# Performance work log

Hardware: AMD Instinct MI355X
Metric: run time of the kernel (lower is better)

Reference implementation:

```python
import jax, jax.numpy as jnp
import numpy as np

N = 4096   # atoms
B = 64     # structures in batch
K = 128    # k-vectors per structure
E = 256    # emb_size_atom
D = 8      # downprojection_size
NUM_HIDDEN = 3


def _silu(x):
    return x * jax.nn.sigmoid(x)


def _residual(x, W):
    # ResidualLayer: two bias-free Dense(E,E) with SiLU, plus skip
    y = _silu(x @ W[0].T)
    y = _silu(y @ W[1].T)
    return x + y


def setup_inputs() -> dict:
    key = jax.random.key(0)
    ks = jax.random.split(key, 10)
    h = jax.random.normal(ks[0], (N, E), jnp.float32)
    x = jax.random.uniform(ks[1], (N, 3), jnp.float32) * 10.0  # Angstrom-scale positions
    k = jax.random.normal(ks[2], (B, K, 3), jnp.float32)
    batch_seg = jnp.sort(jax.random.randint(ks[3], (N,), 0, B))
    sc = 1.0 / np.sqrt(E)
    W_pre = jax.random.normal(ks[4], (2, E, E), jnp.float32) * sc        # pre_residual
    W_down = jax.random.normal(ks[5], (D, K), jnp.float32) / np.sqrt(K)  # shared downprojection (D,K)
    W_up = jax.random.normal(ks[6], (E, D), jnp.float32) / np.sqrt(D)    # up (E,D)
    W0 = jax.random.normal(ks[7], (E, E), jnp.float32) * sc              # first dense of ewald_layers
    W_res = jax.random.normal(ks[8], (NUM_HIDDEN, 2, E, E), jnp.float32) * sc
    return {"h": h, "x": x, "k": k, "batch_seg": batch_seg, "num_batch": B,
            "W_pre": W_pre, "W_down": W_down, "W_up": W_up, "W0": W0, "W_res": W_res}


def reference(h, x, k, batch_seg, num_batch, W_pre, W_down, W_up, W0, W_res):
    hres = _residual(h, W_pre)                       # (N,E)
    # dot products of atom positions with their structure's k-vectors
    dot = jnp.einsum('nkd,nd->nk', k[batch_seg], x)  # (N,K); sinc_damping == 1 (use_pbc)
    c, s = jnp.cos(dot), jnp.sin(dot)
    # structure factors: scatter-sum over atoms within each structure
    sf_real = jax.ops.segment_sum(hres[:, None, :] * c[:, :, None], batch_seg,
                                  num_segments=num_batch)  # (B,K,E)
    sf_imag = jax.ops.segment_sum(hres[:, None, :] * s[:, :, None], batch_seg,
                                  num_segments=num_batch)  # (B,K,E)
    # low-rank learned Fourier-space filter (use_pbc branch)
    kfilter = (W_up @ W_down).T                      # (K,E)
    # re-project filtered structure factors back to atoms
    h_update = 0.01 * jnp.sum(
        (sf_real * kfilter)[batch_seg] * c[:, :, None]
        + (sf_imag * kfilter)[batch_seg] * s[:, :, None], axis=1)  # (N,E)
    # ewald_layers update MLP: Dense + num_hidden residual blocks
    hu = _silu(h_update @ W0.T)
    for i in range(NUM_HIDDEN):
        hu = _residual(hu, W_res[i])
    return hu, dot
```

## Files before the change

### kernel.cpp

```cpp
#include <hip/hip_runtime.h>

#define NN 4096
#define BB 64
#define KK 128
#define EE 256
#define HTS 4352
#define CSR 4224
#define PCAP 160
#define YTS 264
#define ZTS 20

typedef unsigned short u16;
typedef __bf16 bhalf;
typedef bhalf bhalf8 __attribute__((ext_vector_type(8)));
typedef float floatx4 __attribute__((ext_vector_type(4)));

__device__ __forceinline__ float b2f(u16 u) {
  union { unsigned int i; float f; } v; v.i = ((unsigned int)u) << 16; return v.f;
}
__device__ __forceinline__ u16 f2b(float f) {
  union { float f; unsigned int i; } v; v.f = f;
  unsigned int r = (v.i + 0x7FFFu + ((v.i >> 16) & 1u)) >> 16;
  return (u16)r;
}
__device__ __forceinline__ float silu_f(float v) {
  return v / (1.f + __expf(-v));
}


__global__ __launch_bounds__(256) void p1_k(
    const float* __restrict__ h, const float* __restrict__ Wpre,
    const float* __restrict__ W0, const float* __restrict__ Wres,
    const float* __restrict__ Wup, const float* __restrict__ Wdn,
    const int* __restrict__ bs, const float* __restrict__ x,
    const float* __restrict__ kvec,
    u16* __restrict__ hb, u16* __restrict__ wpre, u16* __restrict__ w0b,
    u16* __restrict__ wrb, float* __restrict__ kft, u16* __restrict__ csb,
    int* __restrict__ seg, float* __restrict__ dout)
{
  int bid = blockIdx.x, tid = threadIdx.x;
  if (bid < 4096)      { int i = bid * 256 + tid;          hb[i]   = f2b(h[i]); }
  else if (bid < 6400) {
    int wb = bid - 4096;
    int mat = wb >> 8;
    int o = (wb & 255) * 256 + tid;
    int i = o & 7, lane = (o >> 3) & 63, k = (o >> 9) & 7, nt = o >> 12;
    int r = lane & 15, q = lane >> 4;
    int src = (nt * 16 + r) * 256 + q * 8 + k * 32 + i;
    const float* S; u16* D;
    if (mat < 2)      { S = Wpre + mat * 65536;       D = wpre + mat * 65536; }
    else if (mat == 2){ S = W0;                       D = w0b; }
    else              { S = Wres + (mat - 3) * 65536; D = wrb + (mat - 3) * 65536; }
    D[o] = f2b(S[src]);
  }
  else if (bid < 6528) {
    int i = (bid - 6400) * 256 + tid;
    int e = i >> 7, kk = i & 127;
    float a = 0.f;
#pragma unroll
    for (int d = 0; d < 8; ++d) a += Wup[e * 8 + d] * Wdn[d * KK + kk];
    kft[i] = a;
  } else if (bid < 6656) {
    int i = (bid - 6528) * 256 + tid;
    csb[4096 * 256 + i] = 0;
  } else if (bid == 6656) {
    int b = tid;
    if (b <= BB) {
      int lo = 0, hi = NN;
      while (lo < hi) { int mid = (lo + hi) >> 1; if (bs[mid] < b) lo = mid + 1; else hi = mid; }
      seg[b] = lo;
    }
  } else {
    int i = (bid - 6657) * 256 + tid;
    int n = i >> 7, kk = i & 127;
    int b = bs[n];
    const float* kp = kvec + (b * KK + kk) * 3;
    const float* xp = x + n * 3;
    float d = kp[0] * xp[0] + kp[1] * xp[1] + kp[2] * xp[2];
    float sv, cv;
    sincosf(d, &sv, &cv);
    dout[i] = d;
    csb[(n << 8) + kk] = f2b(cv);
    csb[(n << 8) + 128 + kk] = f2b(sv);
  }
}

__global__ __launch_bounds__(256) void p2_k(
    const u16* __restrict__ X, const u16* __restrict__ Wa, const u16* __restrict__ Wb,
    const float* __restrict__ hskip, u16* __restrict__ ht,
    const u16* __restrict__ csb, const int* __restrict__ seg, u16* __restrict__ ctb)
{
  __shared__ u16 sh[8256];
  if (blockIdx.x < 256) {
    const int lane = threadIdx.x & 63, wv = threadIdx.x >> 6;
    const int m0 = blockIdx.x * 16;
    const int n0 = wv * 64;
    const int r = lane & 15, q = lane >> 4;
    const int lane8 = lane * 8;
    const u16* Ap = X + (m0 + r) * EE + q * 8;
    floatx4 acc[4];
#pragma unroll
    for (int t = 0; t < 4; ++t) acc[t] = (floatx4){0.f, 0.f, 0.f, 0.f};
#pragma unroll
    for (int k = 0; k < 8; ++k) {
      bhalf8 av = *(const bhalf8*)(Ap + k * 32);
#pragma unroll
      for (int t = 0; t < 4; ++t) {
        bhalf8 bv = *(const bhalf8*)(Wa + ((wv * 4 + t) * 8 + k) * 512 + lane8);
        acc[t] = __builtin_amdgcn_mfma_f32_16x16x32_bf16(av, bv, acc[t], 0, 0, 0);
      }
    }
#pragma unroll
    for (int t = 0; t < 4; ++t) {
      int col = n0 + t * 16 + r;
#pragma unroll
      for (int i = 0; i < 4; ++i)
        sh[(q * 4 + i) * YTS + col] = f2b(silu_f(acc[t][i]));
    }
    __syncthreads();
#pragma unroll
    for (int t = 0; t < 4; ++t) acc[t] = (floatx4){0.f, 0.f, 0.f, 0.f};
#pragma unroll
    for (int k = 0; k < 8; ++k) {
      bhalf8 av = *(const bhalf8*)(&sh[r * YTS + q * 8 + k * 32]);
#pragma unroll
      for (int t = 0; t < 4; ++t) {
        bhalf8 bv = *(const bhalf8*)(Wb + ((wv * 4 + t) * 8 + k) * 512 + lane8);
        acc[t] = __builtin_amdgcn_mfma_f32_16x16x32_bf16(av, bv, acc[t], 0, 0, 0);
      }
    }
    __syncthreads();
#pragma unroll
    for (int t = 0; t < 4; ++t) {
      int col = n0 + t * 16 + r;
#pragma unroll
      for (int i = 0; i < 4; ++i) {
        int g = m0 + q * 4 + i;
        float v = silu_f(acc[t][i]) + hskip[g * EE + col];
        sh[col * ZTS + q * 4 + i] = f2b(v);
      }
    }
    __syncthreads();
    int e = threadIdx.x;
    const uint2* src = (const uint2*)&sh[e * ZTS];
    uint2* dst = (uint2*)(ht + e * HTS + m0);
#pragma unroll
    for (int i = 0; i < 4; ++i) dst[i] = src[i];
  } else {
    int bid2 = blockIdx.x - 256;
    int b = bid2 / 5, p0 = (bid2 % 5) * 32, t = threadIdx.x;
    int s0 = seg[b], s1 = seg[b + 1];
    int abase = s0 & ~7;
#pragma unroll
    for (int it = 0; it < 32; ++it) {
      int idx = it * 256 + t;
      int pl = idx >> 8, j = idx & 255;
      int n = abase + p0 + pl;
      u16 v = 0;
      if (n >= s0 && n < s1) v = csb[(n << 8) | j];
      sh[pl * 258 + j] = v;
    }
    __syncthreads();
    unsigned w[16];
#pragma unroll
    for (int i = 0; i < 16; ++i) {
      unsigned lo = sh[(2 * i) * 258 + t];
      unsigned hi = sh[(2 * i + 1) * 258 + t];
      w[i] = lo | (hi << 16);
    }
    uint4* dst = (uint4*)(ctb + ((b << 8) + t) * PCAP + p0);
#pragma unroll
    for (int i = 0; i < 4; ++i) {
      uint4 u; u.x = w[4*i]; u.y = w[4*i+1]; u.z = w[4*i+2]; u.w = w[4*i+3];
      dst[i] = u;
    }
  }
}

__global__ __launch_bounds__(256) void sf_k(
    const u16* __restrict__ ht, const u16* __restrict__ ctb,
    const float* __restrict__ kft, const int* __restrict__ seg, u16* __restrict__ F)
{
  const int lane = threadIdx.x & 63;
  const int wv = threadIdx.x >> 6;
  const int b = blockIdx.x;
  const int e0 = blockIdx.y * 128 + wv * 32;
  const int j0 = blockIdx.z * 64;
  const int r = lane & 15, q = lane >> 4;
  const int abase = seg[b] & ~7;
  const int phi = seg[b + 1] - abase;
  const u16* Ap = ht + (e0 + r) * HTS + abase + q * 8;
  const u16* Bp = ctb + ((b << 8) + j0 + r) * PCAP + q * 8;
  floatx4 acc[2][4];
#pragma unroll
  for (int m = 0; m < 2; ++m)
#pragma unroll
    for (int t = 0; t < 4; ++t) acc[m][t] = (floatx4){0.f, 0.f, 0.f, 0.f};
  for (int p0 = 0; p0 < phi; p0 += 32) {
    bhalf8 a0 = *(const bhalf8*)(Ap + p0);
    bhalf8 a1 = *(const bhalf8*)(Ap + 16 * HTS + p0);
#pragma unroll
    for (int t = 0; t < 4; ++t) {
      bhalf8 bv = *(const bhalf8*)(Bp + t * 16 * PCAP + p0);
      acc[0][t] = __builtin_amdgcn_mfma_f32_16x16x32_bf16(a0, bv, acc[0][t], 0, 0, 0);
      acc[1][t] = __builtin_amdgcn_mfma_f32_16x16x32_bf16(a1, bv, acc[1][t], 0, 0, 0);
    }
  }
#pragma unroll
  for (int m = 0; m < 2; ++m)
#pragma unroll
    for (int t = 0; t < 4; ++t) {
      int col = j0 + t * 16 + r;
      int kk = col & 127;
#pragma unroll
      for (int i = 0; i < 4; ++i) {
        int row = e0 + m * 16 + q * 4 + i;
        F[((b << 8) + row) * 256 + col] = f2b(acc[m][t][i] * kft[row * KK + kk]);
      }
    }
}

__device__ __forceinline__ void stage2(
    const u16* __restrict__ As, const u16* __restrict__ W,
    u16* __restrict__ Ad, const u16* __restrict__ Ask,
    float* __restrict__ outg, int R0, int c0, int r, int q, int wv, int lane8)
{
  bhalf8 a[8];
#pragma unroll
  for (int k = 0; k < 8; ++k)
    a[k] = *(const bhalf8*)(As + r * YTS + q * 8 + k * 32);
  bhalf8 bf[8][2];
#pragma unroll
  for (int k = 0; k < 8; ++k) {
#pragma unroll
    for (int t = 0; t < 2; ++t)
      bf[k][t] = *(const bhalf8*)(W + ((wv * 2 + t) * 8 + k) * 512 + lane8);
  }
  floatx4 acc[2];
  acc[0] = (floatx4){0.f, 0.f, 0.f, 0.f};
  acc[1] = (floatx4){0.f, 0.f, 0.f, 0.f};
#pragma unroll
  for (int k = 0; k < 8; ++k) {
    acc[0] = __builtin_amdgcn_mfma_f32_16x16x32_bf16(a[k], bf[k][0], acc[0], 0, 0, 0);
    acc[1] = __builtin_amdgcn_mfma_f32_16x16x32_bf16(a[k], bf[k][1], acc[1], 0, 0, 0);
  }
#pragma unroll
  for (int t = 0; t < 2; ++t) {
    int col = c0 + t * 16 + r;
#pragma unroll
    for (int i = 0; i < 4; ++i) {
      int row = q * 4 + i;
      float v = silu_f(acc[t][i]);
      if (Ask) v += b2f(Ask[row * YTS + col]);
      if (outg) outg[(R0 + row) * EE + col] = v;
      else      Ad[row * YTS + col] = f2b(v);
    }
  }
}

__global__ __launch_bounds__(512) void tail_k(
    const u16* __restrict__ csb, const u16* __restrict__ F,
    const int* __restrict__ bs, const int* __restrict__ seg,
    const u16* __restrict__ w0b, const u16* __restrict__ wrb,
    float* __restrict__ out)
{
  __shared__ u16 A0[16 * YTS], A1[16 * YTS];
  const int R0 = blockIdx.x * 16;
  const int lane = threadIdx.x & 63, wv = threadIdx.x >> 6;
  const int r = lane & 15, q = lane >> 4;
  const int c0 = wv * 32;
  const int lane8 = lane * 8;
  {
    const u16* Ap = csb + (R0 + r) * 256 + q * 8;
    bhalf8 a[8];
#pragma unroll
    for (int k = 0; k < 8; ++k) a[k] = *(const bhalf8*)(Ap + k * 32);
    int s = bs[R0];
    while (true) {
      const u16* Bp = F + ((s << 8) + c0 + r) * 256 + q * 8;
      bhalf8 bf[8][2];
#pragma unroll
      for (int k = 0; k < 8; ++k) {
        bf[k][0] = *(const bhalf8*)(Bp + k * 32);
        bf[k][1] = *(const bhalf8*)(Bp + 16 * 256 + k * 32);
      }
      floatx4 acc[2];
      acc[0] = (floatx4){0.f, 0.f, 0.f, 0.f};
      acc[1] = (floatx4){0.f, 0.f, 0.f, 0.f};
#pragma unroll
      for (int k = 0; k < 8; ++k) {
        acc[0] = __builtin_amdgcn_mfma_f32_16x16x32_bf16(a[k], bf[k][0], acc[0], 0, 0, 0);
        acc[1] = __builtin_amdgcn_mfma_f32_16x16x32_bf16(a[k], bf[k][1], acc[1], 0, 0, 0);
      }
      int lo = seg[s] - R0;     if (lo < 0)  lo = 0;
      int hi = seg[s + 1] - R0; if (hi > 16) hi = 16;
#pragma unroll
      for (int t = 0; t < 2; ++t) {
        int col = c0 + t * 16 + r;
#pragma unroll
        for (int i = 0; i < 4; ++i) {
          int row = q * 4 + i;
          if (row >= lo && row < hi)
            A0[row * YTS + col] = f2b(0.01f * acc[t][i]);
        }
      }
      if (seg[s + 1] >= R0 + 16) break;
      ++s;
    }
  }
  __syncthreads();
  stage2(A0, w0b,               A1, nullptr, nullptr, R0, c0, r, q, wv, lane8);
  __syncthreads();
  stage2(A1, wrb + 0 * EE * EE, A0, nullptr, nullptr, R0, c0, r, q, wv, lane8);
  __syncthreads();
  stage2(A0, wrb + 1 * EE * EE, A1, A1,      nullptr, R0, c0, r, q, wv, lane8);
  __syncthreads();
  stage2(A1, wrb + 2 * EE * EE, A0, nullptr, nullptr, R0, c0, r, q, wv, lane8);
  __syncthreads();
  stage2(A0, wrb + 3 * EE * EE, A1, A1,      nullptr, R0, c0, r, q, wv, lane8);
  __syncthreads();
  stage2(A1, wrb + 4 * EE * EE, A0, nullptr, nullptr, R0, c0, r, q, wv, lane8);
  __syncthreads();
  stage2(A0, wrb + 5 * EE * EE, nullptr, A1, out,     R0, c0, r, q, wv, lane8);
}

extern "C" void kernel_launch(void* const* d_in, const int* in_sizes, int n_in,
                              void* d_out, int out_size, void* d_ws, size_t ws_size,
                              hipStream_t stream) {
  const float* h    = (const float*)d_in[0];
  const float* x    = (const float*)d_in[1];
  const float* kv   = (const float*)d_in[2];
  const int*   bs   = (const int*)d_in[3];
  const float* Wpre = (const float*)d_in[5];
  const float* Wdn  = (const float*)d_in[6];
  const float* Wup  = (const float*)d_in[7];
  const float* W0   = (const float*)d_in[8];
  const float* Wres = (const float*)d_in[9];
  float* out = (float*)d_out;

  float* kft = (float*)d_ws;
  int*   seg = (int*)(kft + EE * KK);
  u16* hb   = (u16*)(seg + 128);
  u16* wpre = hb + NN * EE;
  u16* w0b  = wpre + 2 * EE * EE;
  u16* wrb  = w0b + EE * EE;
  u16* csb  = wrb + 6 * EE * EE;
  u16* ctb  = csb + CSR * 256;
  u16* ht   = ctb + BB * 256 * PCAP;
  u16* F    = ht + 256 * HTS;

  p1_k<<<8705, 256, 0, stream>>>(h, Wpre, W0, Wres, Wup, Wdn, bs, x, kv,
                                 hb, wpre, w0b, wrb, kft, csb, seg,
                                 out + NN * EE);
  p2_k<<<576, 256, 0, stream>>>(hb, wpre, wpre + EE * EE, h, ht, csb, seg, ctb);
  sf_k<<<dim3(BB, 2, 4), 256, 0, stream>>>(ht, ctb, kft, seg, F);
  tail_k<<<256, 512, 0, stream>>>(csb, F, bs, seg, w0b, wrb, out);
}
```

Before: 125.1 us.

## Fuse h bf16 conversion into GEMM load; double tail row tile and prefetch weights

The separate pass that converts h to bf16 is removed, and p2_k now reads fp32 h and converts it in registers while loading the GEMM operand. The tail kernel processes 32 rows per block instead of 16, so each weight fragment is reused across two M-tiles. The next layer's weights are also prefetched into registers while the current layer's MFMAs run. The trade-offs are higher register pressure, half as many tail blocks (128) for the GPU's CUs, and an extra fp32 read of h in p2.

Measured after the change: 129.3 us. +3.3%, slower.

```diff
diff --git a/kernel.cpp b/kernel.cpp
--- a/kernel.cpp
+++ b/kernel.cpp
@@ -26,24 +26,29 @@
 __device__ __forceinline__ float silu_f(float v) {
   return v / (1.f + __expf(-v));
 }
+__device__ __forceinline__ bhalf8 ld8f(const float* __restrict__ p) {
+  float4 f0 = *(const float4*)p;
+  float4 f1 = *(const float4*)(p + 4);
+  union { bhalf8 v; u16 s[8]; } u;
+  u.s[0] = f2b(f0.x); u.s[1] = f2b(f0.y); u.s[2] = f2b(f0.z); u.s[3] = f2b(f0.w);
+  u.s[4] = f2b(f1.x); u.s[5] = f2b(f1.y); u.s[6] = f2b(f1.z); u.s[7] = f2b(f1.w);
+  return u.v;
+}
 
 
 __global__ __launch_bounds__(256) void p1_k(
-    const float* __restrict__ h, const float* __restrict__ Wpre,
-    const float* __restrict__ W0, const float* __restrict__ Wres,
-    const float* __restrict__ Wup, const float* __restrict__ Wdn,
-    const int* __restrict__ bs, const float* __restrict__ x,
-    const float* __restrict__ kvec,
-    u16* __restrict__ hb, u16* __restrict__ wpre, u16* __restrict__ w0b,
-    u16* __restrict__ wrb, float* __restrict__ kft, u16* __restrict__ csb,
+    const float* __restrict__ Wpre, const float* __restrict__ W0,
+    const float* __restrict__ Wres, const float* __restrict__ Wup,
+    const float* __restrict__ Wdn, const int* __restrict__ bs,
+    const float* __restrict__ x, const float* __restrict__ kvec,
+    u16* __restrict__ wpre, u16* __restrict__ w0b, u16* __restrict__ wrb,
+    float* __restrict__ kft, u16* __restrict__ csb,
     int* __restrict__ seg, float* __restrict__ dout)
 {
   int bid = blockIdx.x, tid = threadIdx.x;
-  if (bid < 4096)      { int i = bid * 256 + tid;          hb[i]   = f2b(h[i]); }
-  else if (bid < 6400) {
-    int wb = bid - 4096;
-    int mat = wb >> 8;
-    int o = (wb & 255) * 256 + tid;
+  if (bid < 2304) {
+    int mat = bid >> 8;
+    int o = (bid & 255) * 256 + tid;
     int i = o & 7, lane = (o >> 3) & 63, k = (o >> 9) & 7, nt = o >> 12;
     int r = lane & 15, q = lane >> 4;
     int src = (nt * 16 + r) * 256 + q * 8 + k * 32 + i;
@@ -53,17 +58,17 @@
     else              { S = Wres + (mat - 3) * 65536; D = wrb + (mat - 3) * 65536; }
     D[o] = f2b(S[src]);
   }
-  else if (bid < 6528) {
-    int i = (bid - 6400) * 256 + tid;
+  else if (bid < 2432) {
+    int i = (bid - 2304) * 256 + tid;
     int e = i >> 7, kk = i & 127;
     float a = 0.f;
 #pragma unroll
     for (int d = 0; d < 8; ++d) a += Wup[e * 8 + d] * Wdn[d * KK + kk];
     kft[i] = a;
-  } else if (bid < 6656) {
-    int i = (bid - 6528) * 256 + tid;
+  } else if (bid < 2560) {
+    int i = (bid - 2432) * 256 + tid;
     csb[4096 * 256 + i] = 0;
-  } else if (bid == 6656) {
+  } else if (bid == 2560) {
     int b = tid;
     if (b <= BB) {
       int lo = 0, hi = NN;
@@ -71,7 +76,7 @@
       seg[b] = lo;
     }
   } else {
-    int i = (bid - 6657) * 256 + tid;
+    int i = (bid - 2561) * 256 + tid;
     int n = i >> 7, kk = i & 127;
     int b = bs[n];
     const float* kp = kvec + (b * KK + kk) * 3;
@@ -86,8 +91,8 @@
 }
 
 __global__ __launch_bounds__(256) void p2_k(
-    const u16* __restrict__ X, const u16* __restrict__ Wa, const u16* __restrict__ Wb,
-    const float* __restrict__ hskip, u16* __restrict__ ht,
+    const float* __restrict__ h, const u16* __restrict__ Wa, const u16* __restrict__ Wb,
+    u16* __restrict__ ht,
     const u16* __restrict__ csb, const int* __restrict__ seg, u16* __restrict__ ctb)
 {
   __shared__ u16 sh[8256];
@@ -97,13 +102,13 @@
     const int n0 = wv * 64;
     const int r = lane & 15, q = lane >> 4;
     const int lane8 = lane * 8;
-    const u16* Ap = X + (m0 + r) * EE + q * 8;
+    const float* Ap = h + (m0 + r) * EE + q * 8;
     floatx4 acc[4];
 #pragma unroll
     for (int t = 0; t < 4; ++t) acc[t] = (floatx4){0.f, 0.f, 0.f, 0.f};
 #pragma unroll
     for (int k = 0; k < 8; ++k) {
-      bhalf8 av = *(const bhalf8*)(Ap + k * 32);
+      bhalf8 av = ld8f(Ap + k * 32);
 #pragma unroll
       for (int t = 0; t < 4; ++t) {
         bhalf8 bv = *(const bhalf8*)(Wa + ((wv * 4 + t) * 8 + k) * 512 + lane8);
@@ -136,7 +141,7 @@
 #pragma unroll
       for (int i = 0; i < 4; ++i) {
         int g = m0 + q * 4 + i;
-        float v = silu_f(acc[t][i]) + hskip[g * EE + col];
+        float v = silu_f(acc[t][i]) + h[g * EE + col];
         sh[col * ZTS + q * 4 + i] = f2b(v);
       }
     }
@@ -220,108 +225,130 @@
     }
 }
 
-__device__ __forceinline__ void stage2(
-    const u16* __restrict__ As, const u16* __restrict__ W,
+__device__ __forceinline__ void loadB(const u16* __restrict__ W, int wv, int lane8,
+                                      bhalf8 (&bf)[8][2]) {
+#pragma unroll
+  for (int k = 0; k < 8; ++k)
+#pragma unroll
+    for (int t = 0; t < 2; ++t)
+      bf[k][t] = *(const bhalf8*)(W + ((wv * 2 + t) * 8 + k) * 512 + lane8);
+}
+
+__device__ __forceinline__ void stage4(
+    const u16* __restrict__ As, const bhalf8 (&B)[8][2],
+    const u16* __restrict__ Wn, bhalf8 (&Bn)[8][2],
     u16* __restrict__ Ad, const u16* __restrict__ Ask,
     float* __restrict__ outg, int R0, int c0, int r, int q, int wv, int lane8)
 {
-  bhalf8 a[8];
-#pragma unroll
-  for (int k = 0; k < 8; ++k)
-    a[k] = *(const bhalf8*)(As + r * YTS + q * 8 + k * 32);
-  bhalf8 bf[8][2];
-#pragma unroll
-  for (int k = 0; k < 8; ++k) {
-#pragma unroll
-    for (int t = 0; t < 2; ++t)
-      bf[k][t] = *(const bhalf8*)(W + ((wv * 2 + t) * 8 + k) * 512 + lane8);
-  }
-  floatx4 acc[2];
-  acc[0] = (floatx4){0.f, 0.f, 0.f, 0.f};
-  acc[1] = (floatx4){0.f, 0.f, 0.f, 0.f};
-#pragma unroll
-  for (int k = 0; k < 8; ++k) {
-    acc[0] = __builtin_amdgcn_mfma_f32_16x16x32_bf16(a[k], bf[k][0], acc[0], 0, 0, 0);
-    acc[1] = __builtin_amdgcn_mfma_f32_16x16x32_bf16(a[k], bf[k][1], acc[1], 0, 0, 0);
-  }
-#pragma unroll
-  for (int t = 0; t < 2; ++t) {
-    int col = c0 + t * 16 + r;
-#pragma unroll
-    for (int i = 0; i < 4; ++i) {
-      int row = q * 4 + i;
-      float v = silu_f(acc[t][i]);
-      if (Ask) v += b2f(Ask[row * YTS + col]);
-      if (outg) outg[(R0 + row) * EE + col] = v;
-      else      Ad[row * YTS + col] = f2b(v);
-    }
-  }
-}
-
-__global__ __launch_bounds__(512) void tail_k(
+  if (Wn) loadB(Wn, wv, lane8, Bn);
+  floatx4 acc[2][2];
+#pragma unroll
+  for (int m = 0; m < 2; ++m) {
+    acc[m][0] = (floatx4){0.f, 0.f, 0.f, 0.f};
+    acc[m][1] = (floatx4){0.f, 0.f, 0.f, 0.f};
+  }
+#pragma unroll
+  for (int m = 0; m < 2; ++m) {
+    bhalf8 a[8];
+#pragma unroll
+    for (int k = 0; k < 8; ++k)
+      a[k] = *(const bhalf8*)(As + (m * 16 + r) * YTS + q * 8 + k * 32);
+#pragma unroll
+    for (int k = 0; k < 8; ++k) {
+      acc[m][0] = __builtin_amdgcn_mfma_f32_16x16x32_bf16(a[k], B[k][0], acc[m][0], 0, 0, 0);
+      acc[m][1] = __builtin_amdgcn_mfma_f32_16x16x32_bf16(a[k], B[k][1], acc[m][1], 0, 0, 0);
+    }
+  }
+#pragma unroll
+  for (int m = 0; m < 2; ++m)
+#pragma unroll
+    for (int t = 0; t < 2; ++t) {
+      int col = c0 + t * 16 + r;
+#pragma unroll
+      for (int i = 0; i < 4; ++i) {
+        int row = m * 16 + q * 4 + i;
+        float v = silu_f(acc[m][t][i]);
+        if (Ask) v += b2f(Ask[row * YTS + col]);
+        if (outg) outg[(R0 + row) * EE + col] = v;
+        else      Ad[row * YTS + col] = f2b(v);
+      }
+    }
+}
+
+__global__ __launch_bounds__(512, 2) void tail_k(
     const u16* __restrict__ csb, const u16* __restrict__ F,
     const int* __restrict__ bs, const int* __restrict__ seg,
     const u16* __restrict__ w0b, const u16* __restrict__ wrb,
     float* __restrict__ out)
 {
-  __shared__ u16 A0[16 * YTS], A1[16 * YTS];
-  const int R0 = blockIdx.x * 16;
+  __shared__ u16 A0[32 * YTS], A1[32 * YTS];
+  const int R0 = blockIdx.x * 32;
   const int lane = threadIdx.x & 63, wv = threadIdx.x >> 6;
   const int r = lane & 15, q = lane >> 4;
   const int c0 = wv * 32;
   const int lane8 = lane * 8;
+  bhalf8 B0[8][2], B1[8][2];
   {
-    const u16* Ap = csb + (R0 + r) * 256 + q * 8;
-    bhalf8 a[8];
-#pragma unroll
-    for (int k = 0; k < 8; ++k) a[k] = *(const bhalf8*)(Ap + k * 32);
+    bhalf8 a[2][8];
+#pragma unroll
+    for (int m = 0; m < 2; ++m)
+#pragma unroll
+      for (int k = 0; k < 8; ++k)
+        a[m][k] = *(const bhalf8*)(csb + (R0 + m * 16 + r) * 256 + q * 8 + k * 32);
     int s = bs[R0];
     while (true) {
-      const u16* Bp = F + ((s << 8) + c0 + r) * 256 + q * 8;
       bhalf8 bf[8][2];
 #pragma unroll
-      for (int k = 0; k < 8; ++k) {
-        bf[k][0] = *(const bhalf8*)(Bp + k * 32);
-        bf[k][1] = *(const bhalf8*)(Bp + 16 * 256 + k * 32);
-      }
-      floatx4 acc[2];
-      acc[0] = (floatx4){0.f, 0.f, 0.f, 0.f};
-      acc[1] = (floatx4){0.f, 0.f, 0.f, 0.f};
-#pragma unroll
-      for (int k = 0; k < 8; ++k) {
-        acc[0] = __builtin_amdgcn_mfma_f32_16x16x32_bf16(a[k], bf[k][0], acc[0], 0, 0, 0);
-        acc[1] = __builtin_amdgcn_mfma_f32_16x16x32_bf16(a[k], bf[k][1], acc[1], 0, 0, 0);
-      }
+      for (int k = 0; k < 8; ++k)
+#pragma unroll
+        for (int t = 0; t < 2; ++t)
+          bf[k][t] = *(const bhalf8*)(F + ((s << 8) + c0 + t * 16 + r) * 256 + q * 8 + k * 32);
+      floatx4 acc[2][2];
+#pragma unroll
+      for (int m = 0; m < 2; ++m) {
+        acc[m][0] = (floatx4){0.f, 0.f, 0.f, 0.f};
+        acc[m][1] = (floatx4){0.f, 0.f, 0.f, 0.f};
+      }
+#pragma unroll
+      for (int k = 0; k < 8; ++k)
+#pragma unroll
+        for (int m = 0; m < 2; ++m) {
+          acc[m][0] = __builtin_amdgcn_mfma_f32_16x16x32_bf16(a[m][k], bf[k][0], acc[m][0], 0, 0, 0);
+          acc[m][1] = __builtin_amdgcn_mfma_f32_16x16x32_bf16(a[m][k], bf[k][1], acc[m][1], 0, 0, 0);
+        }
       int lo = seg[s] - R0;     if (lo < 0)  lo = 0;
-      int hi = seg[s + 1] - R0; if (hi > 16) hi = 16;
-#pragma unroll
-      for (int t = 0; t < 2; ++t) {
-        int col = c0 + t * 16 + r;
-#pragma unroll
-        for (int i = 0; i < 4; ++i) {
-          int row = q * 4 + i;
-          if (row >= lo && row < hi)
-            A0[row * YTS + col] = f2b(0.01f * acc[t][i]);
+      int hi = seg[s + 1] - R0; if (hi > 32) hi = 32;
+#pragma unroll
+      for (int m = 0; m < 2; ++m)
+#pragma unroll
+        for (int t = 0; t < 2; ++t) {
+          int col = c0 + t * 16 + r;
+#pragma unroll
+          for (int i = 0; i < 4; ++i) {
+            int row = m * 16 + q * 4 + i;
+            if (row >= lo && row < hi)
+              A0[row * YTS + col] = f2b(0.01f * acc[m][t][i]);
+          }
         }
-      }
-      if (seg[s + 1] >= R0 + 16) break;
+      if (seg[s + 1] >= R0 + 32) break;
       ++s;
     }
   }
-  __syncthreads();
-  stage2(A0, w0b,               A1, nullptr, nullptr, R0, c0, r, q, wv, lane8);
-  __syncthreads();
-  stage2(A1, wrb + 0 * EE * EE, A0, nullptr, nullptr, R0, c0, r, q, wv, lane8);
-  __syncthreads();
-  stage2(A0, wrb + 1 * EE * EE, A1, A1,      nullptr, R0, c0, r, q, wv, lane8);
-  __syncthreads();
-  stage2(A1, wrb + 2 * EE * EE, A0, nullptr, nullptr, R0, c0, r, q, wv, lane8);
-  __syncthreads();
-  stage2(A0, wrb + 3 * EE * EE, A1, A1,      nullptr, R0, c0, r, q, wv, lane8);
-  __syncthreads();
-  stage2(A1, wrb + 4 * EE * EE, A0, nullptr, nullptr, R0, c0, r, q, wv, lane8);
-  __syncthreads();
-  stage2(A0, wrb + 5 * EE * EE, nullptr, A1, out,     R0, c0, r, q, wv, lane8);
+  loadB(w0b, wv, lane8, B0);
+  __syncthreads();
+  stage4(A0, B0, wrb + 0 * EE * EE, B1, A1, nullptr, nullptr, R0, c0, r, q, wv, lane8);
+  __syncthreads();
+  stage4(A1, B1, wrb + 1 * EE * EE, B0, A0, nullptr, nullptr, R0, c0, r, q, wv, lane8);
+  __syncthreads();
+  stage4(A0, B0, wrb + 2 * EE * EE, B1, A1, A1,      nullptr, R0, c0, r, q, wv, lane8);
+  __syncthreads();
+  stage4(A1, B1, wrb + 3 * EE * EE, B0, A0, nullptr, nullptr, R0, c0, r, q, wv, lane8);
+  __syncthreads();
+  stage4(A0, B0, wrb + 4 * EE * EE, B1, A1, A1,      nullptr, R0, c0, r, q, wv, lane8);
+  __syncthreads();
+  stage4(A1, B1, wrb + 5 * EE * EE, B0, A0, nullptr, nullptr, R0, c0, r, q, wv, lane8);
+  __syncthreads();
+  stage4(A0, B0, nullptr,           B1, nullptr, A1, out,     R0, c0, r, q, wv, lane8);
 }
 
 extern "C" void kernel_launch(void* const* d_in, const int* in_sizes, int n_in,
@@ -340,8 +367,7 @@
 
   float* kft = (float*)d_ws;
   int*   seg = (int*)(kft + EE * KK);
-  u16* hb   = (u16*)(seg + 128);
-  u16* wpre = hb + NN * EE;
+  u16* wpre = (u16*)(seg + 128);
   u16* w0b  = wpre + 2 * EE * EE;
   u16* wrb  = w0b + EE * EE;
   u16* csb  = wrb + 6 * EE * EE;
@@ -349,10 +375,9 @@
   u16* ht   = ctb + BB * 256 * PCAP;
   u16* F    = ht + 256 * HTS;
 
-  p1_k<<<8705, 256, 0, stream>>>(h, Wpre, W0, Wres, Wup, Wdn, bs, x, kv,
-                                 hb, wpre, w0b, wrb, kft, csb, seg,
-                                 out + NN * EE);
-  p2_k<<<576, 256, 0, stream>>>(hb, wpre, wpre + EE * EE, h, ht, csb, seg, ctb);
+  p1_k<<<4609, 256, 0, stream>>>(Wpre, W0, Wres, Wup, Wdn, bs, x, kv,
+                                 wpre, w0b, wrb, kft, csb, seg, out + NN * EE);
+  p2_k<<<576, 256, 0, stream>>>(h, wpre, wpre + EE * EE, ht, csb, seg, ctb);
   sf_k<<<dim3(BB, 2, 4), 256, 0, stream>>>(ht, ctb, kft, seg, F);
-  tail_k<<<256, 512, 0, stream>>>(csb, F, bs, seg, w0b, wrb, out);
-}
+  tail_k<<<128, 512, 0, stream>>>(csb, F, bs, seg, w0b, wrb, out);
+}
```

## Fuse h bf16 conversion into GEMM load, vectorize weight packing, use fast sincos

Applied to the files above, without the earlier changes.

The separate pass that converts h to bf16 in the prep kernel is removed. The first residual GEMM now loads fp32 h directly and converts it in registers, which drops a full write and re-read of the bf16 copy. Weight repacking and zero-fill now write 8 or 16 elements per thread instead of one, cutting the prep kernel's block count sharply. The accurate sincosf is replaced with the __sincosf intrinsic, which risks accuracy loss for large arguments (positions up to 10 times normal k-vectors), and the dot output is unchanged.

Result: no change. 123.5 us (-1.3%).

```diff
diff --git a/kernel.cpp b/kernel.cpp
--- a/kernel.cpp
+++ b/kernel.cpp
@@ -26,44 +26,52 @@
 __device__ __forceinline__ float silu_f(float v) {
   return v / (1.f + __expf(-v));
 }
+__device__ __forceinline__ bhalf8 ld8f(const float* __restrict__ p) {
+  float4 f0 = *(const float4*)p;
+  float4 f1 = *(const float4*)(p + 4);
+  union { bhalf8 v; u16 s[8]; } u;
+  u.s[0] = f2b(f0.x); u.s[1] = f2b(f0.y); u.s[2] = f2b(f0.z); u.s[3] = f2b(f0.w);
+  u.s[4] = f2b(f1.x); u.s[5] = f2b(f1.y); u.s[6] = f2b(f1.z); u.s[7] = f2b(f1.w);
+  return u.v;
+}
 
 
 __global__ __launch_bounds__(256) void p1_k(
-    const float* __restrict__ h, const float* __restrict__ Wpre,
-    const float* __restrict__ W0, const float* __restrict__ Wres,
-    const float* __restrict__ Wup, const float* __restrict__ Wdn,
-    const int* __restrict__ bs, const float* __restrict__ x,
-    const float* __restrict__ kvec,
-    u16* __restrict__ hb, u16* __restrict__ wpre, u16* __restrict__ w0b,
-    u16* __restrict__ wrb, float* __restrict__ kft, u16* __restrict__ csb,
+    const float* __restrict__ Wpre, const float* __restrict__ W0,
+    const float* __restrict__ Wres, const float* __restrict__ Wup,
+    const float* __restrict__ Wdn, const int* __restrict__ bs,
+    const float* __restrict__ x, const float* __restrict__ kvec,
+    u16* __restrict__ wpre, u16* __restrict__ w0b, u16* __restrict__ wrb,
+    float* __restrict__ kft, u16* __restrict__ csb,
     int* __restrict__ seg, float* __restrict__ dout)
 {
   int bid = blockIdx.x, tid = threadIdx.x;
-  if (bid < 4096)      { int i = bid * 256 + tid;          hb[i]   = f2b(h[i]); }
-  else if (bid < 6400) {
-    int wb = bid - 4096;
-    int mat = wb >> 8;
-    int o = (wb & 255) * 256 + tid;
-    int i = o & 7, lane = (o >> 3) & 63, k = (o >> 9) & 7, nt = o >> 12;
+  if (bid < 288) {
+    int mat = bid >> 5;
+    int w8 = ((bid & 31) * 256 + tid);
+    int o = w8 * 8;
+    int lane = w8 & 63, k = (w8 >> 6) & 7, nt = w8 >> 9;
     int r = lane & 15, q = lane >> 4;
-    int src = (nt * 16 + r) * 256 + q * 8 + k * 32 + i;
+    int src = (nt * 16 + r) * 256 + q * 8 + k * 32;
     const float* S; u16* D;
     if (mat < 2)      { S = Wpre + mat * 65536;       D = wpre + mat * 65536; }
     else if (mat == 2){ S = W0;                       D = w0b; }
     else              { S = Wres + (mat - 3) * 65536; D = wrb + (mat - 3) * 65536; }
-    D[o] = f2b(S[src]);
-  }
-  else if (bid < 6528) {
-    int i = (bid - 6400) * 256 + tid;
+    *(bhalf8*)(D + o) = ld8f(S + src);
+  }
+  else if (bid < 416) {
+    int i = (bid - 288) * 256 + tid;
     int e = i >> 7, kk = i & 127;
     float a = 0.f;
 #pragma unroll
     for (int d = 0; d < 8; ++d) a += Wup[e * 8 + d] * Wdn[d * KK + kk];
     kft[i] = a;
-  } else if (bid < 6656) {
-    int i = (bid - 6528) * 256 + tid;
-    csb[4096 * 256 + i] = 0;
-  } else if (bid == 6656) {
+  } else if (bid < 424) {
+    int base = 4096 * 256 + ((bid - 416) * 256 + tid) * 16;
+    uint4 z = {0, 0, 0, 0};
+    *(uint4*)(csb + base) = z;
+    *(uint4*)(csb + base + 8) = z;
+  } else if (bid == 424) {
     int b = tid;
     if (b <= BB) {
       int lo = 0, hi = NN;
@@ -71,14 +79,14 @@
       seg[b] = lo;
     }
   } else {
-    int i = (bid - 6657) * 256 + tid;
+    int i = (bid - 425) * 256 + tid;
     int n = i >> 7, kk = i & 127;
     int b = bs[n];
     const float* kp = kvec + (b * KK + kk) * 3;
     const float* xp = x + n * 3;
     float d = kp[0] * xp[0] + kp[1] * xp[1] + kp[2] * xp[2];
     float sv, cv;
-    sincosf(d, &sv, &cv);
+    __sincosf(d, &sv, &cv);
     dout[i] = d;
     csb[(n << 8) + kk] = f2b(cv);
     csb[(n << 8) + 128 + kk] = f2b(sv);
@@ -86,8 +94,8 @@
 }
 
 __global__ __launch_bounds__(256) void p2_k(
-    const u16* __restrict__ X, const u16* __restrict__ Wa, const u16* __restrict__ Wb,
-    const float* __restrict__ hskip, u16* __restrict__ ht,
+    const float* __restrict__ h, const u16* __restrict__ Wa, const u16* __restrict__ Wb,
+    u16* __restrict__ ht,
     const u16* __restrict__ csb, const int* __restrict__ seg, u16* __restrict__ ctb)
 {
   __shared__ u16 sh[8256];
@@ -97,13 +105,13 @@
     const int n0 = wv * 64;
     const int r = lane & 15, q = lane >> 4;
     const int lane8 = lane * 8;
-    const u16* Ap = X + (m0 + r) * EE + q * 8;
+    const float* Ap = h + (m0 + r) * EE + q * 8;
     floatx4 acc[4];
 #pragma unroll
     for (int t = 0; t < 4; ++t) acc[t] = (floatx4){0.f, 0.f, 0.f, 0.f};
 #pragma unroll
     for (int k = 0; k < 8; ++k) {
-      bhalf8 av = *(const bhalf8*)(Ap + k * 32);
+      bhalf8 av = ld8f(Ap + k * 32);
 #pragma unroll
       for (int t = 0; t < 4; ++t) {
         bhalf8 bv = *(const bhalf8*)(Wa + ((wv * 4 + t) * 8 + k) * 512 + lane8);
@@ -136,7 +144,7 @@
 #pragma unroll
       for (int i = 0; i < 4; ++i) {
         int g = m0 + q * 4 + i;
-        float v = silu_f(acc[t][i]) + hskip[g * EE + col];
+        float v = silu_f(acc[t][i]) + h[g * EE + col];
         sh[col * ZTS + q * 4 + i] = f2b(v);
       }
     }
@@ -340,8 +348,7 @@
 
   float* kft = (float*)d_ws;
   int*   seg = (int*)(kft + EE * KK);
-  u16* hb   = (u16*)(seg + 128);
-  u16* wpre = hb + NN * EE;
+  u16* wpre = (u16*)(seg + 128);
   u16* w0b  = wpre + 2 * EE * EE;
   u16* wrb  = w0b + EE * EE;
   u16* csb  = wrb + 6 * EE * EE;
@@ -349,10 +356,9 @@
   u16* ht   = ctb + BB * 256 * PCAP;
   u16* F    = ht + 256 * HTS;
 
-  p1_k<<<8705, 256, 0, stream>>>(h, Wpre, W0, Wres, Wup, Wdn, bs, x, kv,
-                                 hb, wpre, w0b, wrb, kft, csb, seg,
-                                 out + NN * EE);
-  p2_k<<<576, 256, 0, stream>>>(hb, wpre, wpre + EE * EE, h, ht, csb, seg, ctb);
+  p1_k<<<2473, 256, 0, stream>>>(Wpre, W0, Wres, Wup, Wdn, bs, x, kv,
+                                 wpre, w0b, wrb, kft, csb, seg, out + NN * EE);
+  p2_k<<<576, 256, 0, stream>>>(h, wpre, wpre + EE * EE, ht, csb, seg, ctb);
   sf_k<<<dim3(BB, 2, 4), 256, 0, stream>>>(ht, ctb, kft, seg, F);
   tail_k<<<256, 512, 0, stream>>>(csb, F, bs, seg, w0b, wrb, out);
 }
```
